# Performance work log

Measured on AMD Instinct MI355X. Metric: run time of the kernel, lower is better.

The kernel has to match this reference:

```python
import jax, jax.numpy as jnp
import numpy as np

T, B, D_IN, D_HID, D_OUT = 2048, 64, 256, 256, 256


def setup_inputs() -> dict:
    key = jax.random.key(0)
    k1, k2, k3, k4 = jax.random.split(key, 4)
    s_in = 1.0 / np.sqrt(D_IN)
    s_h = 1.0 / np.sqrt(D_HID)
    return {
        "x": jax.random.normal(k1, (T, B, D_IN), dtype=jnp.float32),
        "h": jnp.zeros((B, D_HID), dtype=jnp.float32),
        "W_in": jax.random.uniform(k2, (D_HID, D_IN), jnp.float32, -s_in, s_in),
        "W_hid": jax.random.uniform(k3, (D_HID, D_HID), jnp.float32, -s_h, s_h),
        "W_out": jax.random.uniform(k4, (D_OUT, D_HID), jnp.float32, -s_h, s_h),
    }


def reference(x, h, W_in, W_hid, W_out):
    # Precompute input projections for all timesteps in one big matmul: [T,B,H]
    x_proj = jnp.einsum("tbi,hi->tbh", x, W_in)

    def step(h_prev, xp_t):
        h_new = jnp.tanh(xp_t + h_prev @ W_hid.T)
        return h_new, h_new

    h_last, hs = jax.lax.scan(step, h, x_proj)  # hs: [T,B,H]
    ys = jnp.einsum("tbh,oh->tbo", hs, W_out).reshape(-1, W_out.shape[0])
    return ys, h_last
```

## Files before the change

### kernel.cpp

```cpp
#include <hip/hip_runtime.h>
#include <hip/hip_bf16.h>

#define TSTEPS 2048
#define NB 64
#define DH 256
#define NBDH (NB * DH)

typedef __attribute__((ext_vector_type(8))) short short8;
typedef __attribute__((ext_vector_type(4))) float f32x4;
typedef __attribute__((ext_vector_type(4))) int i32x4;

#define WSCALE 2032.0f
#define HSCALE 127.0f
#define INVSC (1.0f / (2032.0f * 127.0f))

__device__ __forceinline__ unsigned short f2bf(float f) {
  union { float f; unsigned u; } v; v.f = f;
  unsigned u = v.u;
  u += 0x7FFFu + ((u >> 16) & 1u);
  return (unsigned short)(u >> 16);
}

__device__ __forceinline__ float fast_tanh(float x) {
  float e = __builtin_amdgcn_exp2f(x * 2.885390081777927f);
  return 1.0f - 2.0f * __builtin_amdgcn_rcpf(e + 1.0f);
}

__device__ __forceinline__ int p2c(int p) {
  int q = p & 31;
  return (p & ~31) | ((q & 1) << 4) | (q >> 1);
}

__global__ void cvt_w(const float* __restrict__ win, const float* __restrict__ whid,
                      const float* __restrict__ wout, unsigned short* __restrict__ wbf,
                      char* __restrict__ wq) {
  int i = blockIdx.x * 256 + threadIdx.x;
  int mat = i >> 16, idx = i & 65535;
  int n = idx >> 8, klin = idx & 255;
  if (mat == 0) {
    wbf[idx] = f2bf(win[idx]);
  } else if (mat == 1) {
    wbf[65536 + idx] = f2bf(wout[n * 256 + p2c(klin)]);
  } else {
    float v = whid[n * 256 + p2c(klin)] * WSCALE;
    int q = (int)__builtin_rintf(fminf(fmaxf(v, -127.f), 127.f));
    wq[idx] = (char)q;
  }
}

__global__ __launch_bounds__(256) void gemm_in(
    const float* __restrict__ x, const unsigned short* __restrict__ Wbf,
    float* __restrict__ Cout) {
  const int w = threadIdx.x >> 6, l = threadIdx.x & 63;
  const int m16 = l & 15, kg = l >> 4;
  const long tile0 = ((long)blockIdx.x * 4 + w) * 2;

  short8 afr[2][8];
  for (int ti = 0; ti < 2; ++ti) {
    const float* ar = x + ((tile0 + ti) * 16 + m16) * 256 + kg * 8;
    for (int ks = 0; ks < 8; ++ks) {
      float4 f0 = *(const float4*)(ar + ks * 32);
      float4 f1 = *(const float4*)(ar + ks * 32 + 4);
      short8 s;
      s[0] = (short)f2bf(f0.x); s[1] = (short)f2bf(f0.y);
      s[2] = (short)f2bf(f0.z); s[3] = (short)f2bf(f0.w);
      s[4] = (short)f2bf(f1.x); s[5] = (short)f2bf(f1.y);
      s[6] = (short)f2bf(f1.z); s[7] = (short)f2bf(f1.w);
      afr[ti][ks] = s;
    }
  }
  for (int nt = 0; nt < 16; ++nt) {
    const int n = nt * 16 + m16;
    const unsigned short* wr = Wbf + n * 256 + kg * 8;
    f32x4 acc0 = {0.f, 0.f, 0.f, 0.f}, acc1 = {0.f, 0.f, 0.f, 0.f};
    for (int ks = 0; ks < 8; ++ks) {
      short8 b = *(const short8*)(wr + ks * 32);
      acc0 = __builtin_amdgcn_mfma_f32_16x16x32_bf16(afr[0][ks], b, acc0, 0, 0, 0);
      acc1 = __builtin_amdgcn_mfma_f32_16x16x32_bf16(afr[1][ks], b, acc1, 0, 0, 0);
    }
    for (int r = 0; r < 4; ++r) {
      Cout[(tile0 * 16 + kg * 4 + r) * 256 + n]       = acc0[r];
      Cout[((tile0 + 1) * 16 + kg * 4 + r) * 256 + n] = acc1[r];
    }
  }
}

__global__ __launch_bounds__(512, 2) void rnn_scan(
    const float* __restrict__ xp, const char* __restrict__ Wq,
    const float* __restrict__ h0, unsigned short* __restrict__ hs) {
  __shared__ __align__(16) char hq[2][256];
  const int tid = threadIdx.x, w = tid >> 6, l = tid & 63;
  const int b = blockIdx.x;
  const int m16 = l & 15, kg = l >> 4;

  i32x4 bq[2][4];
  for (int nt = 0; nt < 2; ++nt) {
    const char* wr = Wq + (w * 32 + nt * 16 + m16) * 256 + kg * 16;
    for (int ks = 0; ks < 4; ++ks) bq[nt][ks] = *(const i32x4*)(wr + ks * 64);
  }

  if (tid < 256) {
    float v = fminf(fmaxf(h0[b * 256 + p2c(tid)], -1.f), 1.f) * HSCALE;
    hq[0][tid] = (char)(int)__builtin_rintf(v);
  }
  __syncthreads();

  const int col0 = w * 32 + m16;
  const char* rda = &hq[0][0] + kg * 16;
  const float* xpb = xp + (long)b * 256 + col0;
  unsigned* hsw = (unsigned*)(hs + (long)b * 256 + w * 32 + 2 * m16);

  float xv0[2], xv1[2], xv2[2], xv3[2];
  if (l < 16) {
    xv0[0] = xpb[0];               xv0[1] = xpb[16];
    xv1[0] = xpb[1L * NBDH];       xv1[1] = xpb[1L * NBDH + 16];
    xv2[0] = xpb[2L * NBDH];       xv2[1] = xpb[2L * NBDH + 16];
    xv3[0] = xpb[3L * NBDH];       xv3[1] = xpb[3L * NBDH + 16];
  }

#define MI8(A, B, C) __builtin_amdgcn_mfma_i32_16x16x64_i8(A, B, C, 0, 0, 0)
#define RNN_STEP(T, CUR, XV, PF)                                              \
  {                                                                           \
    const char* ap = rda + (CUR) * 256;                                       \
    i32x4 a0 = *(const i32x4*)(ap);                                           \
    i32x4 a1 = *(const i32x4*)(ap + 64);                                      \
    i32x4 a2 = *(const i32x4*)(ap + 128);                                     \
    i32x4 a3 = *(const i32x4*)(ap + 192);                                     \
    float xq0 = XV[0], xq1 = XV[1];         \
    i32x4 c0 = {0, 0, 0, 0}, c1 = {0, 0, 0, 0};                               \
    if ((PF) && l < 16) {                       \
      const float* q = xpb + (long)((T) + 4) * NBDH;                          \
      XV[0] = q[0]; XV[1] = q[16];                                            \
    }                                                                         \
    c0 = MI8(a0, bq[0][0], c0); c1 = MI8(a0, bq[1][0], c1);                   \
    c0 = MI8(a1, bq[0][1], c0); c1 = MI8(a1, bq[1][1], c1);                   \
    c0 = MI8(a2, bq[0][2], c0); c1 = MI8(a2, bq[1][2], c1);                   \
    c0 = MI8(a3, bq[0][3], c0); c1 = MI8(a3, bq[1][3], c1);                   \
    float z0 = (float)c0[0] * INVSC + xq0;                                    \
    float z1 = (float)c1[0] * INVSC + xq1;                                    \
    float t0 = fast_tanh(z0), t1 = fast_tanh(z1);                             \
    unsigned pk;                                                              \
    asm("v_cvt_pk_bf16_f32 %0, %1, %2" : "=v"(pk) : "v"(t0), "v"(t1));        \
    int q0 = (int)__builtin_rintf(t0 * HSCALE);                               \
    int q1 = (int)__builtin_rintf(t1 * HSCALE);                               \
    unsigned short uq = (unsigned short)((q0 & 0xFF) | ((q1 & 0xFF) << 8));   \
    if (l < 16) {                                                             \
      *(unsigned short*)(&hq[(CUR) ^ 1][w * 32 + 2 * l]) = uq;                \
      hsw[(long)(T) * 8192] = pk;                                             \
    }                                                                         \
    asm volatile("s_waitcnt lgkmcnt(0)" ::: "memory");    \
    __builtin_amdgcn_s_barrier();                                             \
    __builtin_amdgcn_sched_barrier(0);                                        \
  }

#pragma unroll 1
  for (int t = 0; t < TSTEPS - 4; t += 4) {
    RNN_STEP(t, 0, xv0, true);
    RNN_STEP(t + 1, 1, xv1, true);
    RNN_STEP(t + 2, 0, xv2, true);
    RNN_STEP(t + 3, 1, xv3, true);
  }
  RNN_STEP(TSTEPS - 4, 0, xv0, false);
  RNN_STEP(TSTEPS - 3, 1, xv1, false);
  RNN_STEP(TSTEPS - 2, 0, xv2, false);
  RNN_STEP(TSTEPS - 1, 1, xv3, false);
#undef RNN_STEP
#undef MI8
}

__global__ __launch_bounds__(256) void gemm_out(
    const unsigned short* __restrict__ Abf, const unsigned short* __restrict__ Wbf,
    float* __restrict__ Cout) {
  const int w = threadIdx.x >> 6, l = threadIdx.x & 63;
  const int m16 = l & 15, kg = l >> 4;
  const long tile0 = ((long)blockIdx.x * 4 + w) * 2;

  short8 afr[2][8];
  for (int ti = 0; ti < 2; ++ti) {
    const unsigned short* ar = Abf + ((tile0 + ti) * 16 + m16) * 256 + kg * 8;
    for (int ks = 0; ks < 8; ++ks) afr[ti][ks] = *(const short8*)(ar + ks * 32);
  }
  for (int nt = 0; nt < 16; ++nt) {
    const int n = nt * 16 + m16;
    const unsigned short* wr = Wbf + n * 256 + kg * 8;
    f32x4 acc0 = {0.f, 0.f, 0.f, 0.f}, acc1 = {0.f, 0.f, 0.f, 0.f};
    for (int ks = 0; ks < 8; ++ks) {
      short8 b = *(const short8*)(wr + ks * 32);
      acc0 = __builtin_amdgcn_mfma_f32_16x16x32_bf16(afr[0][ks], b, acc0, 0, 0, 0);
      acc1 = __builtin_amdgcn_mfma_f32_16x16x32_bf16(afr[1][ks], b, acc1, 0, 0, 0);
    }
    for (int r = 0; r < 4; ++r) {
      Cout[(tile0 * 16 + kg * 4 + r) * 256 + n]       = acc0[r];
      Cout[((tile0 + 1) * 16 + kg * 4 + r) * 256 + n] = acc1[r];
    }
  }
}

__global__ void hlast_k(const unsigned short* __restrict__ hs, float* __restrict__ hlast) {
  int i = blockIdx.x * 1024 + threadIdx.x;
  int b = i >> 8, p = i & 255;
  unsigned u = (unsigned)hs[(long)(TSTEPS - 1) * NBDH + b * 256 + p] << 16;
  union { unsigned u; float f; } v; v.u = u;
  hlast[b * 256 + p2c(p)] = v.f;
}

extern "C" void kernel_launch(void* const* d_in, const int* in_sizes, int n_in,
                              void* d_out, int out_size, void* d_ws, size_t ws_size,
                              hipStream_t stream) {
  const float* x    = (const float*)d_in[0];
  const float* h0   = (const float*)d_in[1];
  const float* Win  = (const float*)d_in[2];
  const float* Whid = (const float*)d_in[3];
  const float* Wout = (const float*)d_in[4];
  float* ys    = (float*)d_out;
  float* hlast = ys + (long)TSTEPS * NB * 256;

  unsigned short* wbf     = (unsigned short*)d_ws;
  unsigned short* wbf_in  = wbf;
  unsigned short* wbf_out = wbf + 65536;
  char* wq_hid = (char*)d_ws + 262144;
  float* xproj = (float*)((char*)d_ws + 393216);
  unsigned short* hsbuf =
      (unsigned short*)((char*)d_ws + 393216 + (size_t)TSTEPS * NB * 256 * 4);

  cvt_w<<<dim3(768), dim3(256), 0, stream>>>(Win, Whid, Wout, wbf, wq_hid);
  gemm_in<<<dim3(1024), dim3(256), 0, stream>>>(x, wbf_in, xproj);
  rnn_scan<<<dim3(64), dim3(512), 0, stream>>>(xproj, wq_hid, h0, hsbuf);
  gemm_out<<<dim3(1024), dim3(256), 0, stream>>>(hsbuf, wbf_out, ys);
  hlast_k<<<dim3(16), dim3(1024), 0, stream>>>(hsbuf, hlast);
}
```

Measured before the change: 886.9 us.

## Halve scan block to 4 waves, each computing 64 hidden columns per step

```diff
diff --git a/kernel.cpp b/kernel.cpp
--- a/kernel.cpp
+++ b/kernel.cpp
@@ -27,8 +27,8 @@
 }
 
 __device__ __forceinline__ int p2c(int p) {
-  int q = p & 31;
-  return (p & ~31) | ((q & 1) << 4) | (q >> 1);
+  int q = p & 63;
+  return (p & ~63) | ((q & 3) << 4) | (q >> 2);
 }
 
 __global__ void cvt_w(const float* __restrict__ win, const float* __restrict__ whid,
@@ -85,7 +85,7 @@
   }
 }
 
-__global__ __launch_bounds__(512, 2) void rnn_scan(
+__global__ __launch_bounds__(256, 1) void rnn_scan(
     const float* __restrict__ xp, const char* __restrict__ Wq,
     const float* __restrict__ h0, unsigned short* __restrict__ hs) {
   __shared__ __align__(16) char hq[2][256];
@@ -93,29 +93,32 @@
   const int b = blockIdx.x;
   const int m16 = l & 15, kg = l >> 4;
 
-  i32x4 bq[2][4];
-  for (int nt = 0; nt < 2; ++nt) {
-    const char* wr = Wq + (w * 32 + nt * 16 + m16) * 256 + kg * 16;
+  i32x4 bq[4][4];
+  for (int nt = 0; nt < 4; ++nt) {
+    const char* wr = Wq + (w * 64 + nt * 16 + m16) * 256 + kg * 16;
     for (int ks = 0; ks < 4; ++ks) bq[nt][ks] = *(const i32x4*)(wr + ks * 64);
   }
 
-  if (tid < 256) {
+  {
     float v = fminf(fmaxf(h0[b * 256 + p2c(tid)], -1.f), 1.f) * HSCALE;
     hq[0][tid] = (char)(int)__builtin_rintf(v);
   }
   __syncthreads();
 
-  const int col0 = w * 32 + m16;
   const char* rda = &hq[0][0] + kg * 16;
-  const float* xpb = xp + (long)b * 256 + col0;
-  unsigned* hsw = (unsigned*)(hs + (long)b * 256 + w * 32 + 2 * m16);
-
-  float xv0[2], xv1[2], xv2[2], xv3[2];
+  const float* xpb = xp + (long)b * 256 + w * 64 + m16;
+  uint2* hsw = (uint2*)(hs + (long)b * 256 + w * 64 + 4 * m16);
+  unsigned* ldw0 = (unsigned*)&hq[0][w * 64 + 4 * m16];
+  unsigned* ldw1 = (unsigned*)&hq[1][w * 64 + 4 * m16];
+
+  float xv0[4], xv1[4], xv2[4], xv3[4];
   if (l < 16) {
-    xv0[0] = xpb[0];               xv0[1] = xpb[16];
-    xv1[0] = xpb[1L * NBDH];       xv1[1] = xpb[1L * NBDH + 16];
-    xv2[0] = xpb[2L * NBDH];       xv2[1] = xpb[2L * NBDH + 16];
-    xv3[0] = xpb[3L * NBDH];       xv3[1] = xpb[3L * NBDH + 16];
+    for (int nt = 0; nt < 4; ++nt) {
+      xv0[nt] = xpb[nt * 16];
+      xv1[nt] = xpb[1L * NBDH + nt * 16];
+      xv2[nt] = xpb[2L * NBDH + nt * 16];
+      xv3[nt] = xpb[3L * NBDH + nt * 16];
+    }
   }
 
 #define MI8(A, B, C) __builtin_amdgcn_mfma_i32_16x16x64_i8(A, B, C, 0, 0, 0)
@@ -126,27 +129,39 @@
     i32x4 a1 = *(const i32x4*)(ap + 64);                                      \
     i32x4 a2 = *(const i32x4*)(ap + 128);                                     \
     i32x4 a3 = *(const i32x4*)(ap + 192);                                     \
-    float xq0 = XV[0], xq1 = XV[1];         \
-    i32x4 c0 = {0, 0, 0, 0}, c1 = {0, 0, 0, 0};                               \
-    if ((PF) && l < 16) {                       \
+    float xq0 = XV[0], xq1 = XV[1], xq2 = XV[2], xq3 = XV[3];                 \
+    i32x4 c0 = {0,0,0,0}, c1 = {0,0,0,0}, c2 = {0,0,0,0}, c3 = {0,0,0,0};     \
+    if ((PF) && l < 16) {               \
       const float* q = xpb + (long)((T) + 4) * NBDH;                          \
-      XV[0] = q[0]; XV[1] = q[16];                                            \
+      XV[0] = q[0]; XV[1] = q[16]; XV[2] = q[32]; XV[3] = q[48];              \
     }                                                                         \
     c0 = MI8(a0, bq[0][0], c0); c1 = MI8(a0, bq[1][0], c1);                   \
+    c2 = MI8(a0, bq[2][0], c2); c3 = MI8(a0, bq[3][0], c3);                   \
     c0 = MI8(a1, bq[0][1], c0); c1 = MI8(a1, bq[1][1], c1);                   \
+    c2 = MI8(a1, bq[2][1], c2); c3 = MI8(a1, bq[3][1], c3);                   \
     c0 = MI8(a2, bq[0][2], c0); c1 = MI8(a2, bq[1][2], c1);                   \
+    c2 = MI8(a2, bq[2][2], c2); c3 = MI8(a2, bq[3][2], c3);                   \
     c0 = MI8(a3, bq[0][3], c0); c1 = MI8(a3, bq[1][3], c1);                   \
+    c2 = MI8(a3, bq[2][3], c2); c3 = MI8(a3, bq[3][3], c3);                   \
     float z0 = (float)c0[0] * INVSC + xq0;                                    \
     float z1 = (float)c1[0] * INVSC + xq1;                                    \
+    float z2 = (float)c2[0] * INVSC + xq2;                                    \
+    float z3 = (float)c3[0] * INVSC + xq3;                                    \
     float t0 = fast_tanh(z0), t1 = fast_tanh(z1);                             \
-    unsigned pk;                                                              \
-    asm("v_cvt_pk_bf16_f32 %0, %1, %2" : "=v"(pk) : "v"(t0), "v"(t1));        \
+    float t2 = fast_tanh(z2), t3 = fast_tanh(z3);                             \
+    unsigned pk0, pk1;                                                        \
+    asm("v_cvt_pk_bf16_f32 %0, %1, %2" : "=v"(pk0) : "v"(t0), "v"(t1));       \
+    asm("v_cvt_pk_bf16_f32 %0, %1, %2" : "=v"(pk1) : "v"(t2), "v"(t3));       \
     int q0 = (int)__builtin_rintf(t0 * HSCALE);                               \
     int q1 = (int)__builtin_rintf(t1 * HSCALE);                               \
-    unsigned short uq = (unsigned short)((q0 & 0xFF) | ((q1 & 0xFF) << 8));   \
+    int q2 = (int)__builtin_rintf(t2 * HSCALE);                               \
+    int q3 = (int)__builtin_rintf(t3 * HSCALE);                               \
+    unsigned uq = (q0 & 0xFF) | ((q1 & 0xFF) << 8) |                          \
+                  ((q2 & 0xFF) << 16) | ((unsigned)(q3 & 0xFF) << 24);        \
     if (l < 16) {                                                             \
-      *(unsigned short*)(&hq[(CUR) ^ 1][w * 32 + 2 * l]) = uq;                \
-      hsw[(long)(T) * 8192] = pk;                                             \
+      *((CUR) ? ldw0 : ldw1) = uq;                                            \
+      uint2 st; st.x = pk0; st.y = pk1;                                       \
+      hsw[(long)(T) * 4096] = st;                                             \
     }                                                                         \
     asm volatile("s_waitcnt lgkmcnt(0)" ::: "memory");    \
     __builtin_amdgcn_s_barrier();                                             \
@@ -225,7 +240,7 @@
 
   cvt_w<<<dim3(768), dim3(256), 0, stream>>>(Win, Whid, Wout, wbf, wq_hid);
   gemm_in<<<dim3(1024), dim3(256), 0, stream>>>(x, wbf_in, xproj);
-  rnn_scan<<<dim3(64), dim3(512), 0, stream>>>(xproj, wq_hid, h0, hsbuf);
+  rnn_scan<<<dim3(64), dim3(256), 0, stream>>>(xproj, wq_hid, h0, hsbuf);
   gemm_out<<<dim3(1024), dim3(256), 0, stream>>>(hsbuf, wbf_out, ys);
   hlast_k<<<dim3(16), dim3(1024), 0, stream>>>(hsbuf, hlast);
 }
```

After: 984.6 us. +11.0%, slower.

## Fuse output projection into recurrent scan using int8 MFMA on quantized hidden state

Applied to the files above, without the earlier changes.

```diff
diff --git a/kernel.cpp b/kernel.cpp
--- a/kernel.cpp
+++ b/kernel.cpp
@@ -39,12 +39,11 @@
   int n = idx >> 8, klin = idx & 255;
   if (mat == 0) {
     wbf[idx] = f2bf(win[idx]);
-  } else if (mat == 1) {
-    wbf[65536 + idx] = f2bf(wout[n * 256 + p2c(klin)]);
   } else {
-    float v = whid[n * 256 + p2c(klin)] * WSCALE;
+    const float* m = (mat == 1) ? whid : wout;
+    float v = m[n * 256 + p2c(klin)] * WSCALE;
     int q = (int)__builtin_rintf(fminf(fmaxf(v, -127.f), 127.f));
-    wq[idx] = (char)q;
+    wq[(mat - 1) * 65536 + idx] = (char)q;
   }
 }
 
@@ -87,16 +86,20 @@
 
 __global__ __launch_bounds__(512, 2) void rnn_scan(
     const float* __restrict__ xp, const char* __restrict__ Wq,
-    const float* __restrict__ h0, unsigned short* __restrict__ hs) {
+    const float* __restrict__ h0, float* __restrict__ ys,
+    float* __restrict__ hlast) {
   __shared__ __align__(16) char hq[2][256];
   const int tid = threadIdx.x, w = tid >> 6, l = tid & 63;
   const int b = blockIdx.x;
   const int m16 = l & 15, kg = l >> 4;
 
-  i32x4 bq[2][4];
+  i32x4 bq[2][4], by[2][4];
   for (int nt = 0; nt < 2; ++nt) {
     const char* wr = Wq + (w * 32 + nt * 16 + m16) * 256 + kg * 16;
-    for (int ks = 0; ks < 4; ++ks) bq[nt][ks] = *(const i32x4*)(wr + ks * 64);
+    for (int ks = 0; ks < 4; ++ks) {
+      bq[nt][ks] = *(const i32x4*)(wr + ks * 64);
+      by[nt][ks] = *(const i32x4*)(wr + 65536 + ks * 64);
+    }
   }
 
   if (tid < 256) {
@@ -105,10 +108,9 @@
   }
   __syncthreads();
 
-  const int col0 = w * 32 + m16;
   const char* rda = &hq[0][0] + kg * 16;
-  const float* xpb = xp + (long)b * 256 + col0;
-  unsigned* hsw = (unsigned*)(hs + (long)b * 256 + w * 32 + 2 * m16);
+  const float* xpb = xp + (long)b * 256 + w * 32 + m16;
+  float* ysb = ys + (long)b * 256 + w * 32 + l;
 
   float xv0[2], xv1[2], xv2[2], xv3[2];
   if (l < 16) {
@@ -128,7 +130,7 @@
     i32x4 a3 = *(const i32x4*)(ap + 192);                                     \
     float xq0 = XV[0], xq1 = XV[1];         \
     i32x4 c0 = {0, 0, 0, 0}, c1 = {0, 0, 0, 0};                               \
-    if ((PF) && l < 16) {                       \
+    if ((PF) && l < 16) {               \
       const float* q = xpb + (long)((T) + 4) * NBDH;                          \
       XV[0] = q[0]; XV[1] = q[16];                                            \
     }                                                                         \
@@ -136,17 +138,27 @@
     c0 = MI8(a1, bq[0][1], c0); c1 = MI8(a1, bq[1][1], c1);                   \
     c0 = MI8(a2, bq[0][2], c0); c1 = MI8(a2, bq[1][2], c1);                   \
     c0 = MI8(a3, bq[0][3], c0); c1 = MI8(a3, bq[1][3], c1);                   \
+    i32x4 y0 = {0, 0, 0, 0}, y1 = {0, 0, 0, 0};   \
+    y0 = MI8(a0, by[0][0], y0); y1 = MI8(a0, by[1][0], y1);                   \
+    y0 = MI8(a1, by[0][1], y0); y1 = MI8(a1, by[1][1], y1);                   \
+    y0 = MI8(a2, by[0][2], y0); y1 = MI8(a2, by[1][2], y1);                   \
+    y0 = MI8(a3, by[0][3], y0); y1 = MI8(a3, by[1][3], y1);                   \
     float z0 = (float)c0[0] * INVSC + xq0;                                    \
     float z1 = (float)c1[0] * INVSC + xq1;                                    \
     float t0 = fast_tanh(z0), t1 = fast_tanh(z1);                             \
-    unsigned pk;                                                              \
-    asm("v_cvt_pk_bf16_f32 %0, %1, %2" : "=v"(pk) : "v"(t0), "v"(t1));        \
     int q0 = (int)__builtin_rintf(t0 * HSCALE);                               \
     int q1 = (int)__builtin_rintf(t1 * HSCALE);                               \
     unsigned short uq = (unsigned short)((q0 & 0xFF) | ((q1 & 0xFF) << 8));   \
     if (l < 16) {                                                             \
       *(unsigned short*)(&hq[(CUR) ^ 1][w * 32 + 2 * l]) = uq;                \
-      hsw[(long)(T) * 8192] = pk;                                             \
+      if ((T) > 0) {                                                          \
+        ysb[(long)((T) - 1) * NBDH]      = (float)y0[0] * INVSC;              \
+        ysb[(long)((T) - 1) * NBDH + 16] = (float)y1[0] * INVSC;              \
+      }                                                                       \
+      if ((T) == TSTEPS - 1) {                                                \
+        hlast[b * 256 + w * 32 + l]      = t0;                                \
+        hlast[b * 256 + w * 32 + 16 + l] = t1;                                \
+      }                                                                       \
     }                                                                         \
     asm volatile("s_waitcnt lgkmcnt(0)" ::: "memory");    \
     __builtin_amdgcn_s_barrier();                                             \
@@ -165,43 +177,24 @@
   RNN_STEP(TSTEPS - 2, 0, xv2, false);
   RNN_STEP(TSTEPS - 1, 1, xv3, false);
 #undef RNN_STEP
+
+  {
+    const char* ap = rda;
+    i32x4 a0 = *(const i32x4*)(ap);
+    i32x4 a1 = *(const i32x4*)(ap + 64);
+    i32x4 a2 = *(const i32x4*)(ap + 128);
+    i32x4 a3 = *(const i32x4*)(ap + 192);
+    i32x4 y0 = {0, 0, 0, 0}, y1 = {0, 0, 0, 0};
+    y0 = MI8(a0, by[0][0], y0); y1 = MI8(a0, by[1][0], y1);
+    y0 = MI8(a1, by[0][1], y0); y1 = MI8(a1, by[1][1], y1);
+    y0 = MI8(a2, by[0][2], y0); y1 = MI8(a2, by[1][2], y1);
+    y0 = MI8(a3, by[0][3], y0); y1 = MI8(a3, by[1][3], y1);
+    if (l < 16) {
+      ysb[(long)(TSTEPS - 1) * NBDH]      = (float)y0[0] * INVSC;
+      ysb[(long)(TSTEPS - 1) * NBDH + 16] = (float)y1[0] * INVSC;
+    }
+  }
 #undef MI8
-}
-
-__global__ __launch_bounds__(256) void gemm_out(
-    const unsigned short* __restrict__ Abf, const unsigned short* __restrict__ Wbf,
-    float* __restrict__ Cout) {
-  const int w = threadIdx.x >> 6, l = threadIdx.x & 63;
-  const int m16 = l & 15, kg = l >> 4;
-  const long tile0 = ((long)blockIdx.x * 4 + w) * 2;
-
-  short8 afr[2][8];
-  for (int ti = 0; ti < 2; ++ti) {
-    const unsigned short* ar = Abf + ((tile0 + ti) * 16 + m16) * 256 + kg * 8;
-    for (int ks = 0; ks < 8; ++ks) afr[ti][ks] = *(const short8*)(ar + ks * 32);
-  }
-  for (int nt = 0; nt < 16; ++nt) {
-    const int n = nt * 16 + m16;
-    const unsigned short* wr = Wbf + n * 256 + kg * 8;
-    f32x4 acc0 = {0.f, 0.f, 0.f, 0.f}, acc1 = {0.f, 0.f, 0.f, 0.f};
-    for (int ks = 0; ks < 8; ++ks) {
-      short8 b = *(const short8*)(wr + ks * 32);
-      acc0 = __builtin_amdgcn_mfma_f32_16x16x32_bf16(afr[0][ks], b, acc0, 0, 0, 0);
-      acc1 = __builtin_amdgcn_mfma_f32_16x16x32_bf16(afr[1][ks], b, acc1, 0, 0, 0);
-    }
-    for (int r = 0; r < 4; ++r) {
-      Cout[(tile0 * 16 + kg * 4 + r) * 256 + n]       = acc0[r];
-      Cout[((tile0 + 1) * 16 + kg * 4 + r) * 256 + n] = acc1[r];
-    }
-  }
-}
-
-__global__ void hlast_k(const unsigned short* __restrict__ hs, float* __restrict__ hlast) {
-  int i = blockIdx.x * 1024 + threadIdx.x;
-  int b = i >> 8, p = i & 255;
-  unsigned u = (unsigned)hs[(long)(TSTEPS - 1) * NBDH + b * 256 + p] << 16;
-  union { unsigned u; float f; } v; v.u = u;
-  hlast[b * 256 + p2c(p)] = v.f;
 }
 
 extern "C" void kernel_launch(void* const* d_in, const int* in_sizes, int n_in,
@@ -215,17 +208,11 @@
   float* ys    = (float*)d_out;
   float* hlast = ys + (long)TSTEPS * NB * 256;
 
-  unsigned short* wbf     = (unsigned short*)d_ws;
-  unsigned short* wbf_in  = wbf;
-  unsigned short* wbf_out = wbf + 65536;
-  char* wq_hid = (char*)d_ws + 262144;
-  float* xproj = (float*)((char*)d_ws + 393216);
-  unsigned short* hsbuf =
-      (unsigned short*)((char*)d_ws + 393216 + (size_t)TSTEPS * NB * 256 * 4);
-
-  cvt_w<<<dim3(768), dim3(256), 0, stream>>>(Win, Whid, Wout, wbf, wq_hid);
+  unsigned short* wbf_in = (unsigned short*)d_ws;
+  char* wq = (char*)d_ws + 131072;
+  float* xproj = (float*)((char*)d_ws + 262144);
+
+  cvt_w<<<dim3(768), dim3(256), 0, stream>>>(Win, Whid, Wout, wbf_in, wq);
   gemm_in<<<dim3(1024), dim3(256), 0, stream>>>(x, wbf_in, xproj);
-  rnn_scan<<<dim3(64), dim3(512), 0, stream>>>(xproj, wq_hid, h0, hsbuf);
-  gemm_out<<<dim3(1024), dim3(256), 0, stream>>>(hsbuf, wbf_out, ys);
-  hlast_k<<<dim3(16), dim3(1024), 0, stream>>>(hsbuf, hlast);
-}
+  rnn_scan<<<dim3(64), dim3(512), 0, stream>>>(xproj, wq, h0, ys, hlast);
+}
```

New measurement: 954.9 us. 7.7% more time.
